# Performance work log

Measured on AMD Instinct MI355X. Metric: run time of the kernel, lower is better.

The kernel has to match this reference:

```python
import jax, jax.numpy as jnp
import numpy as np

EPS = 1e-5
B, C, H, W, MIP, CQ = 2, 256, 64, 64, 8, 32  # MIP = max(8, C//32); CQ = C//8


def _bn(x, p):
    # inference BatchNorm; p is [4, C] = (gamma, beta, running_mean, running_var)
    g, b, m, v = p[0], p[1], p[2], p[3]
    s = g / jnp.sqrt(v + EPS)
    return x * s[None, :, None, None] + (b - m * s)[None, :, None, None]


def _c1(x, w):  # 1x1 conv, w: [O, I]
    return jnp.einsum('bchw,oc->bohw', x, w)


def _c3(x, w):  # 3x3 conv, SAME padding, w: [O, I, 3, 3]
    return jax.lax.conv_general_dilated(x, w, (1, 1), 'SAME',
                                        dimension_numbers=('NCHW', 'OIHW', 'NCHW'))


def _cbs1(x, w, p):  # Conv(1x1)+BN+SiLU (YOLOv7 Conv block)
    return jax.nn.silu(_bn(_c1(x, w), p))


def _cbs3(x, w, p):  # Conv(3x3)+BN+SiLU
    return jax.nn.silu(_bn(_c3(x, w), p))


def _maxpool(x, k):  # MaxPool2d(kernel=k, stride=1, padding=k//2)
    p = k // 2
    return jax.lax.reduce_window(x, -jnp.inf, jax.lax.max,
                                 (1, 1, k, k), (1, 1, 1, 1),
                                 ((0, 0), (0, 0), (p, p), (p, p)))


def setup_inputs() -> dict:
    ks = iter(jax.random.split(jax.random.key(0), 64))

    def rn(shape, scale):
        return jax.random.normal(next(ks), shape, jnp.float32) * scale

    def w_(o, i, k=1):  # fan-in scaled conv weight
        sc = 1.0 / float(np.sqrt(i * k * k))
        return rn((o, i) if k == 1 else (o, i, k, k), sc)

    def bnp(c):  # gamma, beta, running_mean, running_var (var > 0)
        return jnp.stack([1.0 + rn((c,), 0.05), rn((c,), 0.05), rn((c,), 0.05),
                          0.5 + jax.random.uniform(next(ks), (c,), jnp.float32)])

    cm = C  # SPPCSPC hidden: int(2*C*0.5) = C
    return dict(
        x=rn((B, C, H, W), 1.0),
        ca_w1=w_(MIP, C), ca_b1=rn((MIP,), 0.05), ca_bn=bnp(MIP),
        ca_wh=w_(C, MIP), ca_bh=rn((C,), 0.05),
        ca_ww=w_(C, MIP), ca_bw=rn((C,), 0.05),
        s1_w=w_(cm, C), s1_bn=bnp(cm),
        s2_w=w_(cm, C), s2_bn=bnp(cm),
        s3_w=w_(cm, cm, 3), s3_bn=bnp(cm),
        s4_w=w_(cm, cm), s4_bn=bnp(cm),
        s5_w=w_(cm, 4 * cm), s5_bn=bnp(cm),
        s6_w=w_(cm, cm, 3), s6_bn=bnp(cm),
        s7_w=w_(C, 2 * cm), s7_bn=bnp(C),
        pq_w=w_(CQ, C), pq_b=rn((CQ,), 0.05),
        pk_w=w_(CQ, C), pk_b=rn((CQ,), 0.05),
        pv_w=w_(C, C), pv_b=rn((C,), 0.05),
        gamma_pa=rn((1,), 1.0), gamma_ca=rn((1,), 1.0),
    )


def reference(x, ca_w1, ca_b1, ca_bn, ca_wh, ca_bh, ca_ww, ca_bw,
              s1_w, s1_bn, s2_w, s2_bn, s3_w, s3_bn, s4_w, s4_bn,
              s5_w, s5_bn, s6_w, s6_bn, s7_w, s7_bn,
              pq_w, pq_b, pk_w, pk_b, pv_w, pv_b, gamma_pa, gamma_ca):
    b, c, h, w = x.shape
    # ---- CoordAtt ----
    xh = jnp.mean(x, axis=3, keepdims=True)                                 # b,c,h,1
    xw = jnp.transpose(jnp.mean(x, axis=2, keepdims=True), (0, 1, 3, 2))    # b,c,w,1
    y = jnp.concatenate([xh, xw], axis=2)                                   # b,c,h+w,1
    y = _bn(_c1(y, ca_w1) + ca_b1[None, :, None, None], ca_bn)
    y = y * jnp.clip(y + 3.0, 0.0, 6.0) / 6.0                               # h_swish
    a_h = jax.nn.sigmoid(_c1(y[:, :, :h], ca_wh) + ca_bh[None, :, None, None])
    a_w = jax.nn.sigmoid(_c1(jnp.transpose(y[:, :, h:], (0, 1, 3, 2)), ca_ww)
                         + ca_bw[None, :, None, None])
    r = x * a_w * a_h
    # ---- SPPCSPC ----
    x1 = _cbs1(_cbs3(_cbs1(r, s1_w, s1_bn), s3_w, s3_bn), s4_w, s4_bn)
    cat = jnp.concatenate([x1] + [_maxpool(x1, k) for k in (5, 9, 13)], axis=1)
    y1 = _cbs3(_cbs1(cat, s5_w, s5_bn), s6_w, s6_bn)
    y2 = _cbs1(r, s2_w, s2_bn)
    res = _cbs1(jnp.concatenate([y1, y2], axis=1), s7_w, s7_bn)
    # ---- PAM (spatial attention) ----
    n = h * w
    f = res.reshape(b, c, n)
    q = jnp.einsum('bcn,oc->bon', f, pq_w) + pq_b[None, :, None]            # b,c/8,n
    k = jnp.einsum('bcn,oc->bon', f, pk_w) + pk_b[None, :, None]
    v = jnp.einsum('bcn,oc->bon', f, pv_w) + pv_b[None, :, None]            # b,c,n
    attn = jax.nn.softmax(jnp.einsum('bcn,bcm->bnm', q, k), axis=-1)        # b,n,n
    res_pa = gamma_pa * jnp.einsum('bcm,bnm->bcn', v, attn).reshape(b, c, h, w) + res
    # ---- CAM (channel attention) ----
    e = jnp.einsum('bcn,bdn->bcd', f, f)                                    # b,c,c
    attn_c = jax.nn.softmax(jnp.max(e, axis=-1, keepdims=True) - e, axis=-1)
    res_ca = gamma_ca * jnp.einsum('bcd,bdn->bcn', attn_c, f).reshape(b, c, h, w) + res
    return res + res_ca + res_pa
```

## Files before the change

### kernel.cpp

```cpp
#include <hip/hip_runtime.h>

typedef unsigned short u16;
typedef __attribute__((ext_vector_type(8))) short bf16x8;
typedef __attribute__((ext_vector_type(4))) float f32x4;
#define EPSV 1e-5f
#define LOG2E 1.4426950408889634f

__device__ __forceinline__ float b2f(u16 u) {
  union { float f; unsigned int i; } v; v.i = ((unsigned int)u) << 16; return v.f;
}
__device__ __forceinline__ u16 f2b(float f) {
  union { float f; unsigned int i; } v; v.f = f;
  unsigned int r = v.i + 0x7FFFu + ((v.i >> 16) & 1u);
  return (u16)(r >> 16);
}
__device__ __forceinline__ u16 f2b_trunc(float f) {
  union { float f; unsigned int i; } v; v.f = f;
  return (u16)(v.i >> 16);
}
__device__ __forceinline__ float silu_(float z) { return z / (1.f + exp2f(-LOG2E * z)); }

__global__ __launch_bounds__(128) void detect_k(const u16* __restrict__ xp, float* __restrict__ flag) {
  __shared__ int cnt[2];
  int t = threadIdx.x;
// ... 27 lines not shown
      int idx = gid - (s ? a.end[s - 1] : 0);
      if (a.mode[s] == 0) {
        float v = flag ? ((const float*)a.src[s])[idx] : b2f(((const u16*)a.src[s])[idx]);
        wsF[a.dst[s] + idx] = v;
      } else {
        u16 h = flag ? f2b(((const float*)a.src[s])[idx]) : ((const u16*)a.src[s])[idx];
        wsH[a.dst[s] + idx] = h;
      }
      return;
    }
  }
}

__global__ __launch_bounds__(256) void w3t(const float* __restrict__ Wsrc, u16* __restrict__ Wdst) {
  int idx = blockIdx.x * 256 + threadIdx.x;
  int ch = idx & 31;
  int o  = (idx >> 5) & 255;
  int tap = (idx >> 13) % 9;
  int c8 = (idx >> 13) / 9;
  int i = c8 * 32 + ch;
  Wdst[idx] = f2b(Wsrc[((long)o * 256 + i) * 9 + tap]);
}

__global__ __launch_bounds__(256) void cvtb(const float* __restrict__ src, u16* __restrict__ dst, int n8) {
  int i = blockIdx.x * 256 + threadIdx.x;
  if (i >= n8) return;
  float4 f0 = *(const float4*)(src + (long)i * 8);
  float4 f1 = *(const float4*)(src + (long)i * 8 + 4);
  union { u16 h[8]; uint4 q; } u;
  u.h[0]=f2b(f0.x); u.h[1]=f2b(f0.y); u.h[2]=f2b(f0.z); u.h[3]=f2b(f0.w);
  u.h[4]=f2b(f1.x); u.h[5]=f2b(f1.y); u.h[6]=f2b(f1.z); u.h[7]=f2b(f1.w);
  *(uint4*)(dst + (long)i * 8) = u.q;
}


__global__ __launch_bounds__(256) void plane_means(const float* __restrict__ x, float* __restrict__ yin) {
  __shared__ float pl[4096];
  int bc = blockIdx.x, t = threadIdx.x;
  const float* xp = x + (long)bc * 4096;
  for (int j = 0; j < 16; ++j) { int id = j * 256 + t; pl[id] = xp[id]; }
  __syncthreads();
  if (t < 64) {
    float s = 0.f;
    for (int w = 0; w < 64; ++w) s += pl[t * 64 + w];
    yin[(long)bc * 128 + t] = s * (1.f / 64.f);
  } else if (t < 128) {
    int w = t - 64; float s = 0.f;
    for (int h = 0; h < 64; ++h) s += pl[h * 64 + w];
    yin[(long)bc * 128 + 64 + w] = s * (1.f / 64.f);
  }
}

__global__ __launch_bounds__(128) void ca_conv1(const float* __restrict__ yin, const float* __restrict__ w1,
                                                const float* __restrict__ b1, const float* __restrict__ bnp,
                                                float* __restrict__ ybn) {
  int b = blockIdx.x, p = threadIdx.x;
  float acc[8] = {0.f,0.f,0.f,0.f,0.f,0.f,0.f,0.f};
  for (int c = 0; c < 256; ++c) {
    float yv = yin[((long)b * 256 + c) * 128 + p];
    #pragma unroll
    for (int o = 0; o < 8; ++o) acc[o] += w1[o * 256 + c] * yv;
  }
  #pragma unroll
  for (int o = 0; o < 8; ++o) {
    float z = acc[o] + b1[o];
    float g = bnp[o], bt = bnp[8 + o], mn = bnp[16 + o], vr = bnp[24 + o];
    float s = g * rsqrtf(vr + EPSV);
    z = z * s + (bt - mn * s);
    float hs = fminf(fmaxf(z + 3.f, 0.f), 6.f) * (1.f / 6.f);
    ybn[((long)b * 8 + o) * 128 + p] = z * hs;
  }
}

__global__ __launch_bounds__(128) void ca_gate(const float* __restrict__ ybn,
    const float* __restrict__ wh, const float* __restrict__ bh,
    const float* __restrict__ ww, const float* __restrict__ bw,
    float* __restrict__ ah, float* __restrict__ aw_) {
  int c = blockIdx.x, b = blockIdx.y, t = threadIdx.x;
  if (t < 64) {
    float d = 0.f;
    #pragma unroll
    for (int o = 0; o < 8; ++o) d += wh[c * 8 + o] * ybn[((long)b * 8 + o) * 128 + t];
    d += bh[c];
    ah[((long)b * 256 + c) * 64 + t] = 1.f / (1.f + exp2f(-LOG2E * d));
  } else {
    int w = t - 64;
    float d = 0.f;
    #pragma unroll
    for (int o = 0; o < 8; ++o) d += ww[c * 8 + o] * ybn[((long)b * 8 + o) * 128 + 64 + w];
    d += bw[c];
    aw_[((long)b * 256 + c) * 64 + w] = 1.f / (1.f + exp2f(-LOG2E * d));
  }
}

__global__ __launch_bounds__(256) void apply_ca(const float* __restrict__ x, const float* __restrict__ ah,
                                                const float* __restrict__ aw_, u16* __restrict__ r) {
  int idx = blockIdx.x * 256 + threadIdx.x;
  int n = idx & 4095, bc = idx >> 12;
  int h = n >> 6, w = n & 63;
  r[idx] = f2b(x[idx] * ah[bc * 64 + h] * aw_[bc * 64 + w]);
}


template<int ACT, int OUTH>
__global__ __launch_bounds__(256) void mfma_cbs(
    const u16* __restrict__ Wbf, long aBS,
    const u16* __restrict__ In, long bBS,
    void* __restrict__ Out, long oBS,
    int O, int K, int N,
    const float* __restrict__ bnp, const float* __restrict__ bias)
{
  __shared__ u16 Bs[2][64 * 40];
  __shared__ float albe[64][2];
  const int t = threadIdx.x;
  const int n0 = blockIdx.x * 64;
  const int o0 = blockIdx.y * 64;
  const int b  = blockIdx.z;
  const int w = t >> 6, l = t & 63, lq = l >> 4, lr = l & 15;
  const int wo = (w >> 1) * 32, wn = (w & 1) * 32;
  if (t < 64) {
    int o = o0 + t;
    float al = 1.f, be = 0.f;
    if (bnp) {
      float g = bnp[o], bt = bnp[O + o], mn = bnp[2 * O + o], vr = bnp[3 * O + o];
      al = g * rsqrtf(vr + EPSV); be = bt - mn * al;
    }
    if (bias) be += bias[o];
    albe[t][0] = al; albe[t][1] = be;
  }
  const u16* Ab = Wbf + (long)b * aBS;
  const u16* inb = In + (long)b * bBS + n0;
  const u16* a0p = Ab + (long)(o0 + wo + lr) * K + lq * 8;
  const u16* a1p = a0p + (long)16 * K;
// ... 12 lines not shown
  for (int kc = 0; kc < K; kc += 32) {
    const int p = (kc >> 5) & 1;
    {
      union { uint4 q; u16 h[8]; } tb; tb.q = b0;
      #pragma unroll
      for (int j = 0; j < 8; ++j) Bs[p ^ 1][(bn8 + j) * 40 + bk] = tb.h[j];
    }
    int kn = kc + 32; if (kn >= K) kn = 0;
    int kb = kc + 64; if (kb >= K) kb = 0;
    uint4 a0n = *(const uint4*)(a0p + kn);
    uint4 a1n = *(const uint4*)(a1p + kn);
    uint4 b0n = *(const uint4*)(inb + (long)(kb + bk) * N + bn8);
    bf16x8 bfv0 = *(const bf16x8*)&Bs[p][(wn + lr) * 40 + lq * 8];
    bf16x8 bfv1 = *(const bf16x8*)&Bs[p][(wn + 16 + lr) * 40 + lq * 8];
    acc[0][0] = __builtin_amdgcn_mfma_f32_16x16x32_bf16(*(const bf16x8*)&a0, bfv0, acc[0][0], 0, 0, 0);
    acc[0][1] = __builtin_amdgcn_mfma_f32_16x16x32_bf16(*(const bf16x8*)&a0, bfv1, acc[0][1], 0, 0, 0);
    acc[1][0] = __builtin_amdgcn_mfma_f32_16x16x32_bf16(*(const bf16x8*)&a1, bfv0, acc[1][0], 0, 0, 0);
    acc[1][1] = __builtin_amdgcn_mfma_f32_16x16x32_bf16(*(const bf16x8*)&a1, bfv1, acc[1][1], 0, 0, 0);
    a0 = a0n; a1 = a1n; b0 = b0n;
    __syncthreads();
  }
  float* ob = (float*)Out + (long)b * oBS;
  u16* obh = (u16*)Out + (long)b * oBS;
  #pragma unroll
  for (int i = 0; i < 2; ++i) {
    #pragma unroll
    for (int r = 0; r < 4; ++r) {
      int ol = wo + i * 16 + lq * 4 + r;
      float al = albe[ol][0], be = albe[ol][1];
      #pragma unroll
      for (int j = 0; j < 2; ++j) {
        float vv = acc[i][j][r] * al + be;
        if (ACT) vv = silu_(vv);
        if (OUTH == 2) {
          int col = n0 + wn + j * 16 + lr;
          obh[((long)(col >> 5) * 256 + (o0 + ol)) * 32 + (col & 31)] = f2b(vv);
        } else if (OUTH) {
          obh[(long)(o0 + ol) * N + n0 + wn + j * 16 + lr] = f2b(vv);
        } else {
          ob[(long)(o0 + ol) * N + n0 + wn + j * 16 + lr] = vv;
        }
      }
    }
  }
}

__global__ __launch_bounds__(256) void conv3_mfma(
    const u16* __restrict__ Wt,
    const u16* __restrict__ In, long iBS,
    u16* __restrict__ Out, long oBS, int O, int I,
    const float* __restrict__ bnp)
{
  __shared__ u16 Bs[2][3 * 66 * 34];
  __shared__ float albe[64][2];
  const int t = threadIdx.x;
  const int h0 = blockIdx.x;
  const int o0 = blockIdx.y * 64;
  const int b  = blockIdx.z;
  const int w = t >> 6, l = t & 63, lq = l >> 4, lr = l & 15;
  const int wn = w * 16;
  if (t < 64) {
    int o = o0 + t;
    float g = bnp[o], bt = bnp[O + o], mn = bnp[2 * O + o], vr = bnp[3 * O + o];
// ... 103 lines not shown
  for (int j = 0; j < 16; ++j) A[r + 2][c0 + 2 + j] = b2f(base[r * 64 + c0 + j]);
  const long CNu = 1048576;
  #pragma unroll 1
  for (int s = 1; s <= 3; ++s) {
    __syncthreads();
    #pragma unroll
    for (int j = 0; j < 16; ++j) {
      int cc = c0 + j;
      float m = fmaxf(fmaxf(fmaxf(A[r+2][cc], A[r+2][cc+1]), fmaxf(A[r+2][cc+2], A[r+2][cc+3])), A[r+2][cc+4]);
      Bb[r + 2][cc + 2] = m;
    }
    __syncthreads();
    u16* out = base + (long)s * CNu;
    #pragma unroll
    for (int j = 0; j < 16; ++j) {
      int hc = c0 + 2 + j;
      float m = fmaxf(fmaxf(fmaxf(Bb[r][hc], Bb[r+1][hc]), fmaxf(Bb[r+2][hc], Bb[r+3][hc])), Bb[r+4][hc]);
      out[r * 64 + c0 + j] = f2b_trunc(m);
      A[r + 2][hc] = m;
    }
  }
}

__global__ __launch_bounds__(256) void transpose_hh(const u16* __restrict__ in, u16* __restrict__ out) {
  __shared__ u16 tile[32][34];
  int b = blockIdx.z;
  int c0 = blockIdx.x * 32, r0 = blockIdx.y * 32;
  int tx = threadIdx.x & 31, ty = threadIdx.x >> 5;
  const u16* ib = in + (long)b * 262144;
  u16* ob = out + (long)b * 262144;
  #pragma unroll
  for (int i = 0; i < 4; ++i) {
    int r = r0 + ty + i * 8;
    tile[ty + i * 8][tx] = ib[(long)r * 4096 + c0 + tx];
  }
  __syncthreads();
  #pragma unroll
  for (int i = 0; i < 4; ++i) {
    int c = c0 + ty + i * 8;
    ob[(long)c * 64 + r0 + tx] = tile[tx][ty + i * 8];
  }
}

__global__ __launch_bounds__(256) void pam_qk_max(const u16* __restrict__ qkT, float* __restrict__ pmax) {
  __shared__ u16 Qs[32 * 40];
  __shared__ u16 Ks[2][64 * 40];
  __shared__ float red[4][32][17];
  const int t = threadIdx.x;
  const int b = blockIdx.z, ms = blockIdx.y, n0 = blockIdx.x * 32;
  const int w = t >> 6, l = t & 63, lq = l >> 4, lr = l & 15;
  const int wn = w & 1, wc = w >> 1;
  if (t < 128) {
    int row = t >> 2, cq = (t & 3) * 8;
    *(uint4*)&Qs[row * 40 + cq] = *(const uint4*)(qkT + ((long)b * 4096 + n0 + row) * 64 + cq);
  }
  const int krow = t >> 2, kcq = (t & 3) * 8;
  const u16* kb = qkT + ((long)b * 4096 + krow) * 64 + 32 + kcq;
  {
    uint4 k0 = *(const uint4*)(kb + (long)(ms * 1024) * 64);
    *(uint4*)&Ks[0][krow * 40 + kcq] = k0;
  }
  uint4 kreg = *(const uint4*)(kb + (long)(ms * 1024 + 64) * 64);
  __syncthreads();
  bf16x8 qf = *(const bf16x8*)&Qs[(wn * 16 + lr) * 40 + lq * 8];
  float mx4[4] = {-1e30f, -1e30f, -1e30f, -1e30f};
  for (int it = 0; it < 16; ++it) {
    const int p = it & 1;
    *(uint4*)&Ks[p ^ 1][krow * 40 + kcq] = kreg;
    int itn = it + 2; if (itn >= 16) itn = 0;
    kreg = *(const uint4*)(kb + (long)(ms * 1024 + itn * 64) * 64);
    #pragma unroll
    for (int s = 0; s < 2; ++s) {
      int msub = wc * 2 + s;
      bf16x8 kf = *(const bf16x8*)&Ks[p][(msub * 16 + lr) * 40 + lq * 8];
      f32x4 S = {};
      S = __builtin_amdgcn_mfma_f32_16x16x32_bf16(qf, kf, S, 0, 0, 0);
      #pragma unroll
      for (int r = 0; r < 4; ++r) mx4[r] = fmaxf(mx4[r], S[r]);
    }
    __syncthreads();
  }
  #pragma unroll
  for (int r = 0; r < 4; ++r) red[w][wn * 16 + lq * 4 + r][lr] = mx4[r];
  __syncthreads();
  if (t < 32) {
    int wbase = t >> 4;
    float M = -1e30f;
    #pragma unroll
    for (int j = 0; j < 2; ++j)
      #pragma unroll
      for (int l2 = 0; l2 < 16; ++l2)
        M = fmaxf(M, red[wbase + 2 * j][t][l2]);
    pmax[((long)ms * 2 + b) * 4096 + n0 + t] = M;
  }
}

__global__ __launch_bounds__(256) void pam_merge(const float* __restrict__ pmax, float* __restrict__ rmx) {
  int i = blockIdx.x * 256 + threadIdx.x;
  int b = i >> 12, n = i & 4095;
  float m = pmax[(long)b * 4096 + n];
  #pragma unroll
  for (int ms = 1; ms < 4; ++ms) m = fmaxf(m, pmax[((long)ms * 2 + b) * 4096 + n]);
  rmx[i] = m;
}

__global__ __launch_bounds__(512) void pam_attn(const u16* __restrict__ qkT,
    const u16* __restrict__ vb, const float* __restrict__ rowmax,
    float* __restrict__ Obase, float* __restrict__ Sbase) {
  __shared__ u16 Qs[32 * 40];
  __shared__ u16 Ks[2][64 * 40];
  __shared__ u16 Ps[2][32 * 72];
  __shared__ float rmL[32];
  __shared__ float srow[32];
  const int t = threadIdx.x;
  const int mh = blockIdx.y;
  const int b = blockIdx.z;
  const int n0 = blockIdx.x * 32;
  const int w = t >> 6, l = t & 63, lq = l >> 4, lr = l & 15;
  const int nf = w & 1;
  const int mf = w >> 1;
  const int cw = w * 32;
  float* O = Obase + (long)mh * 2097152;
  float* S = Sbase + (long)mh * 8192;
  if (t < 128) {
    int row = t >> 2, cq = (t & 3) * 8;
    *(uint4*)&Qs[row * 40 + cq] = *(const uint4*)(qkT + ((long)b * 4096 + n0 + row) * 64 + cq);
  }
  if (t < 32) { rmL[t] = rowmax[(long)b * 4096 + n0 + t] * LOG2E; srow[t] = 0.f; }
  const int krow = t >> 3, kc4 = (t & 7) * 4;
  const u16* kbase = qkT + ((long)b * 4096 + krow) * 64 + 32 + kc4;
  const u16* vop = vb + (long)b * 1048576 + (cw + lr) * 32 + lq * 8;
  const int mStart = mh * 2048, mEnd = mStart + 2048;

  {
    uint2 k0 = *(const uint2*)(kbase + (long)mStart * 64);
    *(uint2*)&Ks[0][krow * 40 + kc4] = k0;
  }
  uint2 kreg = *(const uint2*)(kbase + (long)(mStart + 64) * 64);
  long vt0 = (long)(mStart >> 5) * 8192;
  uint4 vA00 = *(const uint4*)(vop + vt0);
  uint4 vA01 = *(const uint4*)(vop + vt0 + 512);
  uint4 vA10 = *(const uint4*)(vop + vt0 + 8192);
  uint4 vA11 = *(const uint4*)(vop + vt0 + 8704);
  uint4 vB00, vB01, vB10, vB11;

  __syncthreads();
  bf16x8 qf = *(const bf16x8*)&Qs[(nf * 16 + lr) * 40 + lq * 8];
  const float rml = rmL[nf * 16 + lr];
  float spl = 0.f;
  f32x4 acc[2][2] = {};

#define QK_PHASE(KBUF, PBUF)                                                   \
  {                                                                            \
    bf16x8 kf = *(const bf16x8*)&Ks[KBUF][(mf * 16 + lr) * 40 + lq * 8];       \
    f32x4 Sv = {};                                                             \
    Sv = __builtin_amdgcn_mfma_f32_16x16x32_bf16(kf, qf, Sv, 0, 0, 0);         \
    union { u16 h[4]; uint2 q; } pk;                                           \
    _Pragma("unroll")                                                          \
    for (int r = 0; r < 4; ++r) {                                              \
      float p = exp2f(Sv[r] * LOG2E - rml);                                    \
      spl += p;                                                                \
      pk.h[r] = f2b_trunc(p);                                                  \
    }                                                                          \
    *(uint2*)&Ps[PBUF][(nf * 16 + lr) * 72 + mf * 16 + lq * 4] = pk.q;         \
  }

#define PV_PHASE(PBUF, V00, V01, V10, V11)                                     \
  {                                                                            \
    bf16x8 pf0 = *(const bf16x8*)&Ps[PBUF][lr * 72 + lq * 8];                  \
    bf16x8 pf1 = *(const bf16x8*)&Ps[PBUF][(16 + lr) * 72 + lq * 8];           \
    acc[0][0] = __builtin_amdgcn_mfma_f32_16x16x32_bf16(*(bf16x8*)&V00, pf0, acc[0][0], 0, 0, 0); \
    acc[0][1] = __builtin_amdgcn_mfma_f32_16x16x32_bf16(*(bf16x8*)&V00, pf1, acc[0][1], 0, 0, 0); \
    acc[1][0] = __builtin_amdgcn_mfma_f32_16x16x32_bf16(*(bf16x8*)&V01, pf0, acc[1][0], 0, 0, 0); \
    acc[1][1] = __builtin_amdgcn_mfma_f32_16x16x32_bf16(*(bf16x8*)&V01, pf1, acc[1][1], 0, 0, 0); \
    pf0 = *(const bf16x8*)&Ps[PBUF][lr * 72 + 32 + lq * 8];                    \
    pf1 = *(const bf16x8*)&Ps[PBUF][(16 + lr) * 72 + 32 + lq * 8];             \
    acc[0][0] = __builtin_amdgcn_mfma_f32_16x16x32_bf16(*(bf16x8*)&V10, pf0, acc[0][0], 0, 0, 0); \
    acc[0][1] = __builtin_amdgcn_mfma_f32_16x16x32_bf16(*(bf16x8*)&V10, pf1, acc[0][1], 0, 0, 0); \
    acc[1][0] = __builtin_amdgcn_mfma_f32_16x16x32_bf16(*(bf16x8*)&V11, pf0, acc[1][0], 0, 0, 0); \
    acc[1][1] = __builtin_amdgcn_mfma_f32_16x16x32_bf16(*(bf16x8*)&V11, pf1, acc[1][1], 0, 0, 0); \
  }

  #pragma unroll 1
  for (int m0 = mStart; m0 < mEnd; m0 += 128) {
    int m2 = m0 + 128; if (m2 >= mEnd) m2 = mStart;
    int m3 = m0 + 192; if (m3 >= mEnd) m3 = mStart;
    QK_PHASE(0, 0)
    *(uint2*)&Ks[1][krow * 40 + kc4] = kreg;
    kreg = *(const uint2*)(kbase + (long)m2 * 64);
    {
      long vt = (long)((m0 + 64) >> 5) * 8192;
      vB00 = *(const uint4*)(vop + vt);
      vB01 = *(const uint4*)(vop + vt + 512);
      vB10 = *(const uint4*)(vop + vt + 8192);
      vB11 = *(const uint4*)(vop + vt + 8704);
    }
    __syncthreads();
    __builtin_amdgcn_s_setprio(1);
    PV_PHASE(0, vA00, vA01, vA10, vA11)
    __builtin_amdgcn_s_setprio(0);
    QK_PHASE(1, 1)
    *(uint2*)&Ks[0][krow * 40 + kc4] = kreg;
    kreg = *(const uint2*)(kbase + (long)m3 * 64);
    {
      long vt = (long)(m2 >> 5) * 8192;
      vA00 = *(const uint4*)(vop + vt);
      vA01 = *(const uint4*)(vop + vt + 512);
      vA10 = *(const uint4*)(vop + vt + 8192);
      vA11 = *(const uint4*)(vop + vt + 8704);
    }
    __syncthreads();
    __builtin_amdgcn_s_setprio(1);
    PV_PHASE(1, vB00, vB01, vB10, vB11)
    __builtin_amdgcn_s_setprio(0);
  }
#undef QK_PHASE
#undef PV_PHASE

  spl += __shfl_xor(spl, 16);
  spl += __shfl_xor(spl, 32);
  if (l < 16) atomicAdd(&srow[nf * 16 + lr], spl);
  __syncthreads();
  if (t < 32) S[(long)b * 4096 + n0 + t] = srow[t];
  float* ob = O + (long)b * 1048576 + n0;
  #pragma unroll
  for (int cf = 0; cf < 2; ++cf) {
    #pragma unroll
    for (int r = 0; r < 4; ++r) {
      int c = cw + cf * 16 + lq * 4 + r;
      ob[(long)c * 4096 + lr]      = acc[cf][0][r];
      ob[(long)c * 4096 + 16 + lr] = acc[cf][1][r];
    }
  }
}


__global__ __launch_bounds__(256) void fillz(float* __restrict__ p, int n) {
  int i = blockIdx.x * 256 + threadIdx.x;
  if (i < n) p[i] = 0.f;
}

__global__ __launch_bounds__(256) void cam_e_mfma(const u16* __restrict__ resb, float* __restrict__ e) {
  __shared__ u16 Bs[2][128 * 40];
  const int t = threadIdx.x;
  const int d0 = blockIdx.x * 128;
  const int c0 = blockIdx.y * 64;
  const int bz = blockIdx.z;
  const int b = bz >> 4, ks = bz & 15;
  const int w = t >> 6, l = t & 63, lq = l >> 4, lr = l & 15;
  const int wo = (w >> 1) * 32, wn = (w & 1) * 64;
  const u16* fb = resb + (long)b * 1048576;
  const u16* a0p = fb + (long)(c0 + wo + lr) * 4096 + lq * 8;
  const u16* a1p = a0p + (long)16 * 4096;
  const int bo = t >> 1, bkq = (t & 1) * 16;
  const u16* bp = fb + (long)(d0 + bo) * 4096 + bkq;
  const int kS = ks * 256, kE = kS + 256;
  f32x4 acc[2][4] = {};
  uint4 b0 = *(const uint4*)(bp + kS);
  uint4 b1 = *(const uint4*)(bp + kS + 8);
  *(uint4*)&Bs[0][bo * 40 + bkq] = b0;
  *(uint4*)&Bs[0][bo * 40 + bkq + 8] = b1;
  b0 = *(const uint4*)(bp + kS + 32);
  b1 = *(const uint4*)(bp + kS + 40);
  uint4 a0 = *(const uint4*)(a0p + kS);
  uint4 a1 = *(const uint4*)(a1p + kS);
  __syncthreads();
  for (int kc = kS; kc < kE; kc += 32) {
    const int p = ((kc - kS) >> 5) & 1;
    *(uint4*)&Bs[p ^ 1][bo * 40 + bkq] = b0;
    *(uint4*)&Bs[p ^ 1][bo * 40 + bkq + 8] = b1;
    int kn = kc + 32; if (kn >= kE) kn = kS;
    int kb = kc + 64; if (kb >= kE) kb = kS;
    uint4 a0n = *(const uint4*)(a0p + kn);
    uint4 a1n = *(const uint4*)(a1p + kn);
    uint4 b0n = *(const uint4*)(bp + kb);
    uint4 b1n = *(const uint4*)(bp + kb + 8);
    #pragma unroll
    for (int j = 0; j < 4; ++j) {
      bf16x8 bfv = *(const bf16x8*)&Bs[p][(wn + j * 16 + lr) * 40 + lq * 8];
      acc[0][j] = __builtin_amdgcn_mfma_f32_16x16x32_bf16(*(const bf16x8*)&a0, bfv, acc[0][j], 0, 0, 0);
      acc[1][j] = __builtin_amdgcn_mfma_f32_16x16x32_bf16(*(const bf16x8*)&a1, bfv, acc[1][j], 0, 0, 0);
    }
    a0 = a0n; a1 = a1n; b0 = b0n; b1 = b1n;
    __syncthreads();
  }
  #pragma unroll
  for (int i = 0; i < 2; ++i)
    #pragma unroll
    for (int r = 0; r < 4; ++r) {
      int ol = wo + i * 16 + lq * 4 + r;
      #pragma unroll
      for (int j = 0; j < 4; ++j)
        atomicAdd(&e[((long)b << 16) + (long)(c0 + ol) * 256 + d0 + wn + j * 16 + lr], acc[i][j][r]);
    }
}

__global__ __launch_bounds__(256) void cam_softmax(const float* __restrict__ e, u16* __restrict__ attn) {
  __shared__ float red[256];
  int c = blockIdx.x, b = blockIdx.y, t = threadIdx.x;
  const float* row = e + ((long)b << 16) + (long)c * 256;
  float v = row[t];
  red[t] = v; __syncthreads();
  for (int s = 128; s > 0; s >>= 1) { if (t < s) red[t] = fminf(red[t], red[t + s]); __syncthreads(); }
  float emin = red[0]; __syncthreads();
  float ex = exp2f(LOG2E * (emin - v));
  red[t] = ex; __syncthreads();
  for (int s = 128; s > 0; s >>= 1) { if (t < s) red[t] += red[t + s]; __syncthreads(); }
// ... 16 lines not shown
}


extern "C" void kernel_launch(void* const* d_in, const int* in_sizes, int n_in,
                              void* d_out, int out_size, void* d_ws, size_t ws_size,
                              hipStream_t stream)
{
  (void)out_size; (void)ws_size; (void)n_in;
  float* ws = (float*)d_ws;
  const long CN = 1048576;

  float* A  = ws;
  float* Bp = ws + 2 * CN;
  float* Cp = ws + 4 * CN;
  float* D  = ws + 6 * CN;
  const long WFo = 14 * CN;

  u16*   rB   = (u16*)A;
  float* res  = A;
  float* xf   = Bp;
  u16*   BpU  = (u16*)Bp;
  float* yin  = Cp;
  float* ybn  = Cp + 65536;
  float* ah   = Cp + 67584;
  float* aw_  = Cp + 100352;
  u16*   CpU  = (u16*)Cp;
  u16*   catU = (u16*)D;
  u16*   y12U = (u16*)D;
  float* D2   = D + 2 * CN;
  u16*   qkbU = (u16*)D2;
  u16*   qkTU = (u16*)(D2 + 262144);
  float* pmax = D2 + 524288;
  float* rmx  = D2 + 557056;
  float* e    = D2 + 565248;
  u16*   attnc= (u16*)(D2 + 696320);
  float* S0   = D2 + 761856;
  float* cam  = D;
  float* O0   = D + 4 * CN;

  ConvArgs ca;
  long fOff[30], hOff[30];
  long hcur = 0;
  float* flagp = ws + WFo;
  {
    long cum = 0, fcur = WFo + 4;
    for (int i = 0; i < 30; ++i) {
      ca.src[i] = d_in[i];
      int h = (i == 8 || i == 10 || i == 14 || i == 16 || i == 20 ||
               i == 22 || i == 24 || i == 26) ? 1 : 0;
      ca.mode[i] = h;
      if (i == 0) { ca.dst[i] = 2 * CN; fOff[i] = 2 * CN; }
      else if (h) { ca.dst[i] = hcur; hOff[i] = hcur; hcur += in_sizes[i]; }
      else        { ca.dst[i] = fcur; fOff[i] = fcur; fcur += in_sizes[i]; }
// ... 13 lines not shown

  float* ca_w1 = ws + fOff[1];
  float* ca_b1 = ws + fOff[2];
  float* ca_bn = ws + fOff[3];
  float* ca_wh = ws + fOff[4];
  float* ca_bh = ws + fOff[5];
  float* ca_ww = ws + fOff[6];
  float* ca_bw = ws + fOff[7];
  u16*   s1_w  = wsH + hOff[8];   float* s1_bn = ws + fOff[9];
  u16*   s2_w  = wsH + hOff[10];  float* s2_bn = ws + fOff[11];
  float* s3_wf = ws + fOff[12];   float* s3_bn = ws + fOff[13];
  u16*   s4_w  = wsH + hOff[14];  float* s4_bn = ws + fOff[15];
  u16*   s5_w  = wsH + hOff[16];  float* s5_bn = ws + fOff[17];
  float* s6_wf = ws + fOff[18];   float* s6_bn = ws + fOff[19];
  u16*   s7_w  = wsH + hOff[20];  float* s7_bn = ws + fOff[21];
  u16*   qk_w  = wsH + hOff[22];  float* qk_b  = ws + fOff[23];
  u16*   pv_w  = wsH + hOff[26];  float* pv_b  = ws + fOff[27];
  float* gammas = ws + fOff[28];

  w3t<<<dim3(2304), dim3(256), 0, stream>>>(s3_wf, wt3a);
  w3t<<<dim3(2304), dim3(256), 0, stream>>>(s6_wf, wt3b);

  plane_means<<<dim3(512), dim3(256), 0, stream>>>(xf, yin);
  ca_conv1<<<dim3(2), dim3(128), 0, stream>>>(yin, ca_w1, ca_b1, ca_bn, ybn);
  ca_gate<<<dim3(256, 2), dim3(128), 0, stream>>>(ybn, ca_wh, ca_bh, ca_ww, ca_bw, ah, aw_);
  apply_ca<<<dim3(8192), dim3(256), 0, stream>>>(xf, ah, aw_, rB);

  mfma_cbs<1,1><<<dim3(64, 4, 2), dim3(256), 0, stream>>>(s1_w, 0, rB, CN, CpU, CN, 256, 256, 4096, s1_bn, nullptr);
  conv3_mfma<<<dim3(64, 4, 2), dim3(256), 0, stream>>>(wt3a, CpU, CN, BpU, CN, 256, 256, s3_bn);
  mfma_cbs<1,1><<<dim3(64, 4, 2), dim3(256), 0, stream>>>(s4_w, 0, BpU, CN, catU, 4 * CN, 256, 256, 4096, s4_bn, nullptr);

  pool3<<<dim3(256, 2), dim3(256), 0, stream>>>(catU, 4 * CN);

  mfma_cbs<1,1><<<dim3(64, 4, 2), dim3(256), 0, stream>>>(s5_w, 0, catU, 4 * CN, BpU, CN, 256, 1024, 4096, s5_bn, nullptr);
  conv3_mfma<<<dim3(64, 4, 2), dim3(256), 0, stream>>>(wt3b, BpU, CN, y12U, 2 * CN, 256, 256, s6_bn);
  mfma_cbs<1,1><<<dim3(64, 4, 2), dim3(256), 0, stream>>>(s2_w, 0, rB, CN, y12U + CN, 2 * CN, 256, 256, 4096, s2_bn, nullptr);
  mfma_cbs<1,0><<<dim3(64, 4, 2), dim3(256), 0, stream>>>(s7_w, 0, y12U, 2 * CN, res, CN, 256, 512, 4096, s7_bn, nullptr);

  cvtb<<<dim3(1024), dim3(256), 0, stream>>>(res, BpU, 262144);
  mfma_cbs<0,1><<<dim3(64, 1, 2), dim3(256), 0, stream>>>(qk_w, 0, BpU, CN, qkbU, 262144, 64, 256, 4096, nullptr, qk_b);
  mfma_cbs<0,2><<<dim3(64, 4, 2), dim3(256), 0, stream>>>(pv_w, 0, BpU, CN, CpU, CN, 256, 256, 4096, nullptr, pv_b);
  transpose_hh<<<dim3(128, 2, 2), dim3(256), 0, stream>>>(qkbU, qkTU);

  pam_qk_max<<<dim3(128, 4, 2), dim3(256), 0, stream>>>(qkTU, pmax);
  pam_merge<<<dim3(32), dim3(256), 0, stream>>>(pmax, rmx);
  pam_attn<<<dim3(128, 2, 2), dim3(512), 0, stream>>>(qkTU, CpU, rmx, O0, S0);

  fillz<<<dim3(512), dim3(256), 0, stream>>>(e, 131072);
  cam_e_mfma<<<dim3(2, 4, 32), dim3(256), 0, stream>>>(BpU, e);
  cam_softmax<<<dim3(256, 2), dim3(256), 0, stream>>>(e, attnc);
  mfma_cbs<0,0><<<dim3(64, 4, 2), dim3(256), 0, stream>>>(attnc, 65536, BpU, CN, cam, CN, 256, 256, 4096, nullptr, nullptr);

  combine<<<dim3(8192), dim3(256), 0, stream>>>(res, O0, S0, cam, gammas, d_out, flagp);
}
```

Measured before the change: 429.3 us.

## Fuse CA gate into apply, drop cvtb/transpose, load K fragments directly

```diff
diff --git a/kernel.cpp b/kernel.cpp
--- a/kernel.cpp
+++ b/kernel.cpp
@@ -73,17 +73,6 @@
   Wdst[idx] = f2b(Wsrc[((long)o * 256 + i) * 9 + tap]);
 }
 
-__global__ __launch_bounds__(256) void cvtb(const float* __restrict__ src, u16* __restrict__ dst, int n8) {
-  int i = blockIdx.x * 256 + threadIdx.x;
-  if (i >= n8) return;
-  float4 f0 = *(const float4*)(src + (long)i * 8);
-  float4 f1 = *(const float4*)(src + (long)i * 8 + 4);
-  union { u16 h[8]; uint4 q; } u;
-  u.h[0]=f2b(f0.x); u.h[1]=f2b(f0.y); u.h[2]=f2b(f0.z); u.h[3]=f2b(f0.w);
-  u.h[4]=f2b(f1.x); u.h[5]=f2b(f1.y); u.h[6]=f2b(f1.z); u.h[7]=f2b(f1.w);
-  *(uint4*)(dst + (long)i * 8) = u.q;
-}
-
 
 __global__ __launch_bounds__(256) void plane_means(const float* __restrict__ x, float* __restrict__ yin) {
   __shared__ float pl[4096];
@@ -105,51 +94,36 @@
 __global__ __launch_bounds__(128) void ca_conv1(const float* __restrict__ yin, const float* __restrict__ w1,
                                                 const float* __restrict__ b1, const float* __restrict__ bnp,
                                                 float* __restrict__ ybn) {
-  int b = blockIdx.x, p = threadIdx.x;
-  float acc[8] = {0.f,0.f,0.f,0.f,0.f,0.f,0.f,0.f};
-  for (int c = 0; c < 256; ++c) {
-    float yv = yin[((long)b * 256 + c) * 128 + p];
-    #pragma unroll
-    for (int o = 0; o < 8; ++o) acc[o] += w1[o * 256 + c] * yv;
-  }
+  int b = blockIdx.x, o = blockIdx.y, p = threadIdx.x;
+  float acc = 0.f;
+  for (int c = 0; c < 256; ++c)
+    acc += w1[o * 256 + c] * yin[((long)b * 256 + c) * 128 + p];
+  float z = acc + b1[o];
+  float g = bnp[o], bt = bnp[8 + o], mn = bnp[16 + o], vr = bnp[24 + o];
+  float s = g * rsqrtf(vr + EPSV);
+  z = z * s + (bt - mn * s);
+  float hs = fminf(fmaxf(z + 3.f, 0.f), 6.f) * (1.f / 6.f);
+  ybn[((long)b * 8 + o) * 128 + p] = z * hs;
+}
+
+__global__ __launch_bounds__(256) void apply_ca(const float* __restrict__ x, const float* __restrict__ ybn,
+    const float* __restrict__ wh, const float* __restrict__ bh,
+    const float* __restrict__ ww, const float* __restrict__ bw,
+    u16* __restrict__ r) {
+  int idx = blockIdx.x * 256 + threadIdx.x;
+  int n = idx & 4095, bc = idx >> 12;
+  int b = bc >> 8, c = bc & 255;
+  int h = n >> 6, w = n & 63;
+  const float* yb = ybn + (long)b * 1024;
+  float d1 = bh[c], d2 = bw[c];
   #pragma unroll
   for (int o = 0; o < 8; ++o) {
-    float z = acc[o] + b1[o];
-    float g = bnp[o], bt = bnp[8 + o], mn = bnp[16 + o], vr = bnp[24 + o];
-    float s = g * rsqrtf(vr + EPSV);
-    z = z * s + (bt - mn * s);
-    float hs = fminf(fmaxf(z + 3.f, 0.f), 6.f) * (1.f / 6.f);
-    ybn[((long)b * 8 + o) * 128 + p] = z * hs;
-  }
-}
-
-__global__ __launch_bounds__(128) void ca_gate(const float* __restrict__ ybn,
-    const float* __restrict__ wh, const float* __restrict__ bh,
-    const float* __restrict__ ww, const float* __restrict__ bw,
-    float* __restrict__ ah, float* __restrict__ aw_) {
-  int c = blockIdx.x, b = blockIdx.y, t = threadIdx.x;
-  if (t < 64) {
-    float d = 0.f;
-    #pragma unroll
-    for (int o = 0; o < 8; ++o) d += wh[c * 8 + o] * ybn[((long)b * 8 + o) * 128 + t];
-    d += bh[c];
-    ah[((long)b * 256 + c) * 64 + t] = 1.f / (1.f + exp2f(-LOG2E * d));
-  } else {
-    int w = t - 64;
-    float d = 0.f;
-    #pragma unroll
-    for (int o = 0; o < 8; ++o) d += ww[c * 8 + o] * ybn[((long)b * 8 + o) * 128 + 64 + w];
-    d += bw[c];
-    aw_[((long)b * 256 + c) * 64 + w] = 1.f / (1.f + exp2f(-LOG2E * d));
-  }
-}
-
-__global__ __launch_bounds__(256) void apply_ca(const float* __restrict__ x, const float* __restrict__ ah,
-                                                const float* __restrict__ aw_, u16* __restrict__ r) {
-  int idx = blockIdx.x * 256 + threadIdx.x;
-  int n = idx & 4095, bc = idx >> 12;
-  int h = n >> 6, w = n & 63;
-  r[idx] = f2b(x[idx] * ah[bc * 64 + h] * aw_[bc * 64 + w]);
+    d1 += wh[c * 8 + o] * yb[o * 128 + h];
+    d2 += ww[c * 8 + o] * yb[o * 128 + 64 + w];
+  }
+  float ah = 1.f / (1.f + exp2f(-LOG2E * d1));
+  float aw = 1.f / (1.f + exp2f(-LOG2E * d2));
+  r[idx] = f2b(x[idx] * ah * aw);
 }
 
 
@@ -159,7 +133,8 @@
     const u16* __restrict__ In, long bBS,
     void* __restrict__ Out, long oBS,
     int O, int K, int N,
-    const float* __restrict__ bnp, const float* __restrict__ bias)
+    const float* __restrict__ bnp, const float* __restrict__ bias,
+    void* __restrict__ Out2)
 {
   __shared__ u16 Bs[2][64 * 40];
   __shared__ float albe[64][2];
@@ -218,23 +193,45 @@
   }
   float* ob = (float*)Out + (long)b * oBS;
   u16* obh = (u16*)Out + (long)b * oBS;
-  #pragma unroll
-  for (int i = 0; i < 2; ++i) {
-    #pragma unroll
-    for (int r = 0; r < 4; ++r) {
-      int ol = wo + i * 16 + lq * 4 + r;
-      float al = albe[ol][0], be = albe[ol][1];
+  u16* obh2 = Out2 ? (u16*)Out2 + (long)b * oBS : nullptr;
+  if (OUTH == 3) {
+    #pragma unroll
+    for (int i = 0; i < 2; ++i) {
       #pragma unroll
       for (int j = 0; j < 2; ++j) {
-        float vv = acc[i][j][r] * al + be;
-        if (ACT) vv = silu_(vv);
-        if (OUTH == 2) {
-          int col = n0 + wn + j * 16 + lr;
-          obh[((long)(col >> 5) * 256 + (o0 + ol)) * 32 + (col & 31)] = f2b(vv);
-        } else if (OUTH) {
-          obh[(long)(o0 + ol) * N + n0 + wn + j * 16 + lr] = f2b(vv);
-        } else {
-          ob[(long)(o0 + ol) * N + n0 + wn + j * 16 + lr] = vv;
+        int n = n0 + wn + j * 16 + lr;
+        union { u16 h[4]; uint2 q; } pk;
+        #pragma unroll
+        for (int r = 0; r < 4; ++r) {
+          int ol = wo + i * 16 + lq * 4 + r;
+          float vv = acc[i][j][r] * albe[ol][0] + albe[ol][1];
+          if (ACT) vv = silu_(vv);
+          pk.h[r] = f2b(vv);
+        }
+        *(uint2*)&obh[(long)n * 64 + o0 + wo + i * 16 + lq * 4] = pk.q;
+      }
+    }
+  } else {
+    #pragma unroll
+    for (int i = 0; i < 2; ++i) {
+      #pragma unroll
+      for (int r = 0; r < 4; ++r) {
+        int ol = wo + i * 16 + lq * 4 + r;
+        float al = albe[ol][0], be = albe[ol][1];
+        #pragma unroll
+        for (int j = 0; j < 2; ++j) {
+          float vv = acc[i][j][r] * al + be;
+          if (ACT) vv = silu_(vv);
+          if (OUTH == 2) {
+            int col = n0 + wn + j * 16 + lr;
+            obh[((long)(col >> 5) * 256 + (o0 + ol)) * 32 + (col & 31)] = f2b(vv);
+          } else if (OUTH == 1) {
+            obh[(long)(o0 + ol) * N + n0 + wn + j * 16 + lr] = f2b(vv);
+          } else {
+            ob[(long)(o0 + ol) * N + n0 + wn + j * 16 + lr] = vv;
+            if (OUTH == 4)
+              obh2[(long)(o0 + ol) * N + n0 + wn + j * 16 + lr] = f2b(vv);
+          }
         }
       }
     }
@@ -384,63 +381,31 @@
   }
 }
 
-__global__ __launch_bounds__(256) void transpose_hh(const u16* __restrict__ in, u16* __restrict__ out) {
-  __shared__ u16 tile[32][34];
-  int b = blockIdx.z;
-  int c0 = blockIdx.x * 32, r0 = blockIdx.y * 32;
-  int tx = threadIdx.x & 31, ty = threadIdx.x >> 5;
-  const u16* ib = in + (long)b * 262144;
-  u16* ob = out + (long)b * 262144;
-  #pragma unroll
-  for (int i = 0; i < 4; ++i) {
-    int r = r0 + ty + i * 8;
-    tile[ty + i * 8][tx] = ib[(long)r * 4096 + c0 + tx];
-  }
-  __syncthreads();
-  #pragma unroll
-  for (int i = 0; i < 4; ++i) {
-    int c = c0 + ty + i * 8;
-    ob[(long)c * 64 + r0 + tx] = tile[tx][ty + i * 8];
-  }
-}
-
 __global__ __launch_bounds__(256) void pam_qk_max(const u16* __restrict__ qkT, float* __restrict__ pmax) {
-  __shared__ u16 Qs[32 * 40];
-  __shared__ u16 Ks[2][64 * 40];
   __shared__ float red[4][32][17];
   const int t = threadIdx.x;
   const int b = blockIdx.z, ms = blockIdx.y, n0 = blockIdx.x * 32;
   const int w = t >> 6, l = t & 63, lq = l >> 4, lr = l & 15;
   const int wn = w & 1, wc = w >> 1;
-  if (t < 128) {
-    int row = t >> 2, cq = (t & 3) * 8;
-    *(uint4*)&Qs[row * 40 + cq] = *(const uint4*)(qkT + ((long)b * 4096 + n0 + row) * 64 + cq);
-  }
-  const int krow = t >> 2, kcq = (t & 3) * 8;
-  const u16* kb = qkT + ((long)b * 4096 + krow) * 64 + 32 + kcq;
-  {
-    uint4 k0 = *(const uint4*)(kb + (long)(ms * 1024) * 64);
-    *(uint4*)&Ks[0][krow * 40 + kcq] = k0;
-  }
-  uint4 kreg = *(const uint4*)(kb + (long)(ms * 1024 + 64) * 64);
-  __syncthreads();
-  bf16x8 qf = *(const bf16x8*)&Qs[(wn * 16 + lr) * 40 + lq * 8];
+  bf16x8 qf = *(const bf16x8*)(qkT + ((long)b * 4096 + n0 + wn * 16 + lr) * 64 + lq * 8);
+  const u16* kb0 = qkT + ((long)b * 4096 + ms * 1024 + wc * 32 + lr) * 64 + 32 + lq * 8;
+  uint4 k0 = *(const uint4*)(kb0);
+  uint4 k1 = *(const uint4*)(kb0 + 16 * 64);
   float mx4[4] = {-1e30f, -1e30f, -1e30f, -1e30f};
+  #pragma unroll 1
   for (int it = 0; it < 16; ++it) {
-    const int p = it & 1;
-    *(uint4*)&Ks[p ^ 1][krow * 40 + kcq] = kreg;
-    int itn = it + 2; if (itn >= 16) itn = 0;
-    kreg = *(const uint4*)(kb + (long)(ms * 1024 + itn * 64) * 64);
-    #pragma unroll
-    for (int s = 0; s < 2; ++s) {
-      int msub = wc * 2 + s;
-      bf16x8 kf = *(const bf16x8*)&Ks[p][(msub * 16 + lr) * 40 + lq * 8];
-      f32x4 S = {};
-      S = __builtin_amdgcn_mfma_f32_16x16x32_bf16(qf, kf, S, 0, 0, 0);
-      #pragma unroll
-      for (int r = 0; r < 4; ++r) mx4[r] = fmaxf(mx4[r], S[r]);
-    }
-    __syncthreads();
+    int nx = (it + 1) & 15;
+    uint4 k0n = *(const uint4*)(kb0 + (long)nx * 4096);
+    uint4 k1n = *(const uint4*)(kb0 + (long)nx * 4096 + 1024);
+    f32x4 S = {};
+    S = __builtin_amdgcn_mfma_f32_16x16x32_bf16(qf, *(const bf16x8*)&k0, S, 0, 0, 0);
+    #pragma unroll
+    for (int r = 0; r < 4; ++r) mx4[r] = fmaxf(mx4[r], S[r]);
+    f32x4 S2 = {};
+    S2 = __builtin_amdgcn_mfma_f32_16x16x32_bf16(qf, *(const bf16x8*)&k1, S2, 0, 0, 0);
+    #pragma unroll
+    for (int r = 0; r < 4; ++r) mx4[r] = fmaxf(mx4[r], S2[r]);
+    k0 = k0n; k1 = k1n;
   }
   #pragma unroll
   for (int r = 0; r < 4; ++r) red[w][wn * 16 + lq * 4 + r][lr] = mx4[r];
@@ -469,8 +434,6 @@
 __global__ __launch_bounds__(512) void pam_attn(const u16* __restrict__ qkT,
     const u16* __restrict__ vb, const float* __restrict__ rowmax,
     float* __restrict__ Obase, float* __restrict__ Sbase) {
-  __shared__ u16 Qs[32 * 40];
-  __shared__ u16 Ks[2][64 * 40];
   __shared__ u16 Ps[2][32 * 72];
   __shared__ float rmL[32];
   __shared__ float srow[32];
@@ -484,21 +447,14 @@
   const int cw = w * 32;
   float* O = Obase + (long)mh * 2097152;
   float* S = Sbase + (long)mh * 8192;
-  if (t < 128) {
-    int row = t >> 2, cq = (t & 3) * 8;
-    *(uint4*)&Qs[row * 40 + cq] = *(const uint4*)(qkT + ((long)b * 4096 + n0 + row) * 64 + cq);
-  }
   if (t < 32) { rmL[t] = rowmax[(long)b * 4096 + n0 + t] * LOG2E; srow[t] = 0.f; }
-  const int krow = t >> 3, kc4 = (t & 7) * 4;
-  const u16* kbase = qkT + ((long)b * 4096 + krow) * 64 + 32 + kc4;
+  bf16x8 qf = *(const bf16x8*)(qkT + ((long)b * 4096 + n0 + nf * 16 + lr) * 64 + lq * 8);
+  const u16* kfp = qkT + ((long)b * 4096 + mf * 16 + lr) * 64 + 32 + lq * 8;
   const u16* vop = vb + (long)b * 1048576 + (cw + lr) * 32 + lq * 8;
   const int mStart = mh * 2048, mEnd = mStart + 2048;
 
-  {
-    uint2 k0 = *(const uint2*)(kbase + (long)mStart * 64);
-    *(uint2*)&Ks[0][krow * 40 + kc4] = k0;
-  }
-  uint2 kreg = *(const uint2*)(kbase + (long)(mStart + 64) * 64);
+  uint4 kfA = *(const uint4*)(kfp + (long)mStart * 64);
+  uint4 kfB = *(const uint4*)(kfp + (long)(mStart + 64) * 64);
   long vt0 = (long)(mStart >> 5) * 8192;
   uint4 vA00 = *(const uint4*)(vop + vt0);
   uint4 vA01 = *(const uint4*)(vop + vt0 + 512);
@@ -507,16 +463,14 @@
   uint4 vB00, vB01, vB10, vB11;
 
   __syncthreads();
-  bf16x8 qf = *(const bf16x8*)&Qs[(nf * 16 + lr) * 40 + lq * 8];
   const float rml = rmL[nf * 16 + lr];
   float spl = 0.f;
   f32x4 acc[2][2] = {};
 
-#define QK_PHASE(KBUF, PBUF)                                                   \
+#define QK_PHASE(KREG, PBUF)                                                   \
   {                                                                            \
-    bf16x8 kf = *(const bf16x8*)&Ks[KBUF][(mf * 16 + lr) * 40 + lq * 8];       \
     f32x4 Sv = {};                                                             \
-    Sv = __builtin_amdgcn_mfma_f32_16x16x32_bf16(kf, qf, Sv, 0, 0, 0);         \
+    Sv = __builtin_amdgcn_mfma_f32_16x16x32_bf16(*(const bf16x8*)&KREG, qf, Sv, 0, 0, 0); \
     union { u16 h[4]; uint2 q; } pk;                                           \
     _Pragma("unroll")                                                          \
     for (int r = 0; r < 4; ++r) {                                              \
@@ -547,9 +501,8 @@
   for (int m0 = mStart; m0 < mEnd; m0 += 128) {
     int m2 = m0 + 128; if (m2 >= mEnd) m2 = mStart;
     int m3 = m0 + 192; if (m3 >= mEnd) m3 = mStart;
-    QK_PHASE(0, 0)
-    *(uint2*)&Ks[1][krow * 40 + kc4] = kreg;
-    kreg = *(const uint2*)(kbase + (long)m2 * 64);
+    QK_PHASE(kfA, 0)
+    kfA = *(const uint4*)(kfp + (long)m2 * 64);
     {
       long vt = (long)((m0 + 64) >> 5) * 8192;
       vB00 = *(const uint4*)(vop + vt);
@@ -561,9 +514,8 @@
     __builtin_amdgcn_s_setprio(1);
     PV_PHASE(0, vA00, vA01, vA10, vA11)
     __builtin_amdgcn_s_setprio(0);
-    QK_PHASE(1, 1)
-    *(uint2*)&Ks[0][krow * 40 + kc4] = kreg;
-    kreg = *(const uint2*)(kbase + (long)m3 * 64);
+    QK_PHASE(kfB, 1)
+    kfB = *(const uint4*)(kfp + (long)m3 * 64);
     {
       long vt = (long)(m2 >> 5) * 8192;
       vA00 = *(const uint4*)(vop + vt);
@@ -603,48 +555,43 @@
 }
 
 __global__ __launch_bounds__(256) void cam_e_mfma(const u16* __restrict__ resb, float* __restrict__ e) {
-  __shared__ u16 Bs[2][128 * 40];
   const int t = threadIdx.x;
   const int d0 = blockIdx.x * 128;
   const int c0 = blockIdx.y * 64;
   const int bz = blockIdx.z;
-  const int b = bz >> 4, ks = bz & 15;
+  const int b = bz >> 5, ks = bz & 31;
   const int w = t >> 6, l = t & 63, lq = l >> 4, lr = l & 15;
   const int wo = (w >> 1) * 32, wn = (w & 1) * 64;
   const u16* fb = resb + (long)b * 1048576;
   const u16* a0p = fb + (long)(c0 + wo + lr) * 4096 + lq * 8;
   const u16* a1p = a0p + (long)16 * 4096;
-  const int bo = t >> 1, bkq = (t & 1) * 16;
-  const u16* bp = fb + (long)(d0 + bo) * 4096 + bkq;
-  const int kS = ks * 256, kE = kS + 256;
+  const u16* bpl = fb + (long)(d0 + wn + lr) * 4096 + lq * 8;
+  const int kS = ks * 128, kE = kS + 128;
   f32x4 acc[2][4] = {};
-  uint4 b0 = *(const uint4*)(bp + kS);
-  uint4 b1 = *(const uint4*)(bp + kS + 8);
-  *(uint4*)&Bs[0][bo * 40 + bkq] = b0;
-  *(uint4*)&Bs[0][bo * 40 + bkq + 8] = b1;
-  b0 = *(const uint4*)(bp + kS + 32);
-  b1 = *(const uint4*)(bp + kS + 40);
   uint4 a0 = *(const uint4*)(a0p + kS);
   uint4 a1 = *(const uint4*)(a1p + kS);
-  __syncthreads();
+  uint4 b0 = *(const uint4*)(bpl + kS);
+  uint4 b1 = *(const uint4*)(bpl + 16 * 4096 + kS);
+  uint4 b2 = *(const uint4*)(bpl + 32 * 4096 + kS);
+  uint4 b3 = *(const uint4*)(bpl + 48 * 4096 + kS);
+  #pragma unroll 1
   for (int kc = kS; kc < kE; kc += 32) {
-    const int p = ((kc - kS) >> 5) & 1;
-    *(uint4*)&Bs[p ^ 1][bo * 40 + bkq] = b0;
-    *(uint4*)&Bs[p ^ 1][bo * 40 + bkq + 8] = b1;
     int kn = kc + 32; if (kn >= kE) kn = kS;
-    int kb = kc + 64; if (kb >= kE) kb = kS;
     uint4 a0n = *(const uint4*)(a0p + kn);
     uint4 a1n = *(const uint4*)(a1p + kn);
-    uint4 b0n = *(const uint4*)(bp + kb);
-    uint4 b1n = *(const uint4*)(bp + kb + 8);
-    #pragma unroll
-    for (int j = 0; j < 4; ++j) {
-      bf16x8 bfv = *(const bf16x8*)&Bs[p][(wn + j * 16 + lr) * 40 + lq * 8];
-      acc[0][j] = __builtin_amdgcn_mfma_f32_16x16x32_bf16(*(const bf16x8*)&a0, bfv, acc[0][j], 0, 0, 0);
-      acc[1][j] = __builtin_amdgcn_mfma_f32_16x16x32_bf16(*(const bf16x8*)&a1, bfv, acc[1][j], 0, 0, 0);
-    }
-    a0 = a0n; a1 = a1n; b0 = b0n; b1 = b1n;
-    __syncthreads();
+    uint4 b0n = *(const uint4*)(bpl + kn);
+    uint4 b1n = *(const uint4*)(bpl + 16 * 4096 + kn);
+    uint4 b2n = *(const uint4*)(bpl + 32 * 4096 + kn);
+    uint4 b3n = *(const uint4*)(bpl + 48 * 4096 + kn);
+    acc[0][0] = __builtin_amdgcn_mfma_f32_16x16x32_bf16(*(const bf16x8*)&a0, *(const bf16x8*)&b0, acc[0][0], 0, 0, 0);
+    acc[0][1] = __builtin_amdgcn_mfma_f32_16x16x32_bf16(*(const bf16x8*)&a0, *(const bf16x8*)&b1, acc[0][1], 0, 0, 0);
+    acc[0][2] = __builtin_amdgcn_mfma_f32_16x16x32_bf16(*(const bf16x8*)&a0, *(const bf16x8*)&b2, acc[0][2], 0, 0, 0);
+    acc[0][3] = __builtin_amdgcn_mfma_f32_16x16x32_bf16(*(const bf16x8*)&a0, *(const bf16x8*)&b3, acc[0][3], 0, 0, 0);
+    acc[1][0] = __builtin_amdgcn_mfma_f32_16x16x32_bf16(*(const bf16x8*)&a1, *(const bf16x8*)&b0, acc[1][0], 0, 0, 0);
+    acc[1][1] = __builtin_amdgcn_mfma_f32_16x16x32_bf16(*(const bf16x8*)&a1, *(const bf16x8*)&b1, acc[1][1], 0, 0, 0);
+    acc[1][2] = __builtin_amdgcn_mfma_f32_16x16x32_bf16(*(const bf16x8*)&a1, *(const bf16x8*)&b2, acc[1][2], 0, 0, 0);
+    acc[1][3] = __builtin_amdgcn_mfma_f32_16x16x32_bf16(*(const bf16x8*)&a1, *(const bf16x8*)&b3, acc[1][3], 0, 0, 0);
+    a0 = a0n; a1 = a1n; b0 = b0n; b1 = b1n; b2 = b2n; b3 = b3n;
   }
   #pragma unroll
   for (int i = 0; i < 2; ++i)
@@ -707,13 +654,10 @@
   u16*   BpU  = (u16*)Bp;
   float* yin  = Cp;
   float* ybn  = Cp + 65536;
-  float* ah   = Cp + 67584;
-  float* aw_  = Cp + 100352;
   u16*   CpU  = (u16*)Cp;
   u16*   catU = (u16*)D;
   u16*   y12U = (u16*)D;
   float* D2   = D + 2 * CN;
-  u16*   qkbU = (u16*)D2;
   u16*   qkTU = (u16*)(D2 + 262144);
   float* pmax = D2 + 524288;
   float* rmx  = D2 + 557056;
@@ -773,34 +717,31 @@
   w3t<<<dim3(2304), dim3(256), 0, stream>>>(s6_wf, wt3b);
 
   plane_means<<<dim3(512), dim3(256), 0, stream>>>(xf, yin);
-  ca_conv1<<<dim3(2), dim3(128), 0, stream>>>(yin, ca_w1, ca_b1, ca_bn, ybn);
-  ca_gate<<<dim3(256, 2), dim3(128), 0, stream>>>(ybn, ca_wh, ca_bh, ca_ww, ca_bw, ah, aw_);
-  apply_ca<<<dim3(8192), dim3(256), 0, stream>>>(xf, ah, aw_, rB);
-
-  mfma_cbs<1,1><<<dim3(64, 4, 2), dim3(256), 0, stream>>>(s1_w, 0, rB, CN, CpU, CN, 256, 256, 4096, s1_bn, nullptr);
+  ca_conv1<<<dim3(2, 8), dim3(128), 0, stream>>>(yin, ca_w1, ca_b1, ca_bn, ybn);
+  apply_ca<<<dim3(8192), dim3(256), 0, stream>>>(xf, ybn, ca_wh, ca_bh, ca_ww, ca_bw, rB);
+
+  mfma_cbs<1,1><<<dim3(64, 4, 2), dim3(256), 0, stream>>>(s1_w, 0, rB, CN, CpU, CN, 256, 256, 4096, s1_bn, nullptr, nullptr);
   conv3_mfma<<<dim3(64, 4, 2), dim3(256), 0, stream>>>(wt3a, CpU, CN, BpU, CN, 256, 256, s3_bn);
-  mfma_cbs<1,1><<<dim3(64, 4, 2), dim3(256), 0, stream>>>(s4_w, 0, BpU, CN, catU, 4 * CN, 256, 256, 4096, s4_bn, nullptr);
+  mfma_cbs<1,1><<<dim3(64, 4, 2), dim3(256), 0, stream>>>(s4_w, 0, BpU, CN, catU, 4 * CN, 256, 256, 4096, s4_bn, nullptr, nullptr);
 
   pool3<<<dim3(256, 2), dim3(256), 0, stream>>>(catU, 4 * CN);
 
-  mfma_cbs<1,1><<<dim3(64, 4, 2), dim3(256), 0, stream>>>(s5_w, 0, catU, 4 * CN, BpU, CN, 256, 1024, 4096, s5_bn, nullptr);
+  mfma_cbs<1,1><<<dim3(64, 4, 2), dim3(256), 0, stream>>>(s5_w, 0, catU, 4 * CN, BpU, CN, 256, 1024, 4096, s5_bn, nullptr, nullptr);
   conv3_mfma<<<dim3(64, 4, 2), dim3(256), 0, stream>>>(wt3b, BpU, CN, y12U, 2 * CN, 256, 256, s6_bn);
-  mfma_cbs<1,1><<<dim3(64, 4, 2), dim3(256), 0, stream>>>(s2_w, 0, rB, CN, y12U + CN, 2 * CN, 256, 256, 4096, s2_bn, nullptr);
-  mfma_cbs<1,0><<<dim3(64, 4, 2), dim3(256), 0, stream>>>(s7_w, 0, y12U, 2 * CN, res, CN, 256, 512, 4096, s7_bn, nullptr);
-
-  cvtb<<<dim3(1024), dim3(256), 0, stream>>>(res, BpU, 262144);
-  mfma_cbs<0,1><<<dim3(64, 1, 2), dim3(256), 0, stream>>>(qk_w, 0, BpU, CN, qkbU, 262144, 64, 256, 4096, nullptr, qk_b);
-  mfma_cbs<0,2><<<dim3(64, 4, 2), dim3(256), 0, stream>>>(pv_w, 0, BpU, CN, CpU, CN, 256, 256, 4096, nullptr, pv_b);
-  transpose_hh<<<dim3(128, 2, 2), dim3(256), 0, stream>>>(qkbU, qkTU);
+  mfma_cbs<1,1><<<dim3(64, 4, 2), dim3(256), 0, stream>>>(s2_w, 0, rB, CN, y12U + CN, 2 * CN, 256, 256, 4096, s2_bn, nullptr, nullptr);
+  mfma_cbs<1,4><<<dim3(64, 4, 2), dim3(256), 0, stream>>>(s7_w, 0, y12U, 2 * CN, res, CN, 256, 512, 4096, s7_bn, nullptr, BpU);
+
+  mfma_cbs<0,3><<<dim3(64, 1, 2), dim3(256), 0, stream>>>(qk_w, 0, BpU, CN, qkTU, 262144, 64, 256, 4096, nullptr, qk_b, nullptr);
+  mfma_cbs<0,2><<<dim3(64, 4, 2), dim3(256), 0, stream>>>(pv_w, 0, BpU, CN, CpU, CN, 256, 256, 4096, nullptr, pv_b, nullptr);
 
   pam_qk_max<<<dim3(128, 4, 2), dim3(256), 0, stream>>>(qkTU, pmax);
   pam_merge<<<dim3(32), dim3(256), 0, stream>>>(pmax, rmx);
   pam_attn<<<dim3(128, 2, 2), dim3(512), 0, stream>>>(qkTU, CpU, rmx, O0, S0);
 
   fillz<<<dim3(512), dim3(256), 0, stream>>>(e, 131072);
-  cam_e_mfma<<<dim3(2, 4, 32), dim3(256), 0, stream>>>(BpU, e);
+  cam_e_mfma<<<dim3(2, 4, 64), dim3(256), 0, stream>>>(BpU, e);
   cam_softmax<<<dim3(256, 2), dim3(256), 0, stream>>>(e, attnc);
-  mfma_cbs<0,0><<<dim3(64, 4, 2), dim3(256), 0, stream>>>(attnc, 65536, BpU, CN, cam, CN, 256, 256, 4096, nullptr, nullptr);
+  mfma_cbs<0,0><<<dim3(64, 4, 2), dim3(256), 0, stream>>>(attnc, 65536, BpU, CN, cam, CN, 256, 256, 4096, nullptr, nullptr, nullptr);
 
   combine<<<dim3(8192), dim3(256), 0, stream>>>(res, O0, S0, cam, gammas, d_out, flagp);
 }
```

Result: slower. 446.6 us (+4.0%).
